# Optimization experiments

Measured on AMD Instinct MI355X. Metric: run time of the kernel, lower is better.

Reference implementation:

```python
import jax, jax.numpy as jnp
import numpy as np

N = 20000       # nodes
E = 320000      # edges
D_IN = 128
H = 512
OUT = 7
EPS = 1e-5


def setup_inputs() -> dict:
    key = jax.random.key(0)
    ks = jax.random.split(key, 16)
    def lin(k, fan_in, fan_out):
        bound = 1.0 / np.sqrt(fan_in)
        kw, kb = jax.random.split(k)
        W = jax.random.uniform(kw, (fan_in, fan_out), jnp.float32, -bound, bound)
        b = jax.random.uniform(kb, (fan_out,), jnp.float32, -bound, bound)
        return W, b
    x = jax.random.normal(ks[0], (N, D_IN), jnp.float32)
    edge_index = jax.random.randint(ks[1], (2, E), 0, N, dtype=jnp.int64)
    W1, b1 = lin(ks[2], D_IN, H)
    W2, b2 = lin(ks[3], H, H)
    W3, b3 = lin(ks[4], H, H)
    W4, b4 = lin(ks[5], H, H)
    ln_gamma = jnp.ones((H,), jnp.float32)
    ln_beta = jnp.zeros((H,), jnp.float32)
    W_out, b_out = lin(ks[6], H, OUT)
    return {"x": x, "edge_index": edge_index,
            "W1": W1, "b1": b1, "W2": W2, "b2": b2,
            "W3": W3, "b3": b3, "W4": W4, "b4": b4,
            "ln_gamma": ln_gamma, "ln_beta": ln_beta,
            "W_out": W_out, "b_out": b_out}


def _gcn_layer(x, W, b, src, dst, dinv):
    # transform, then symmetric-normalized gather/scatter-add (PyG GCNConv)
    h = x @ W                                    # [N, H]
    norm = dinv[src] * dinv[dst]                 # [E+N]
    msg = h[src] * norm[:, None]                 # gather + scale
    agg = jax.ops.segment_sum(msg, dst, num_segments=N)
    return agg + b


def reference(x, edge_index, W1, b1, W2, b2, W3, b3, W4, b4,
              ln_gamma, ln_beta, W_out, b_out):
    loops = jnp.arange(N, dtype=edge_index.dtype)
    src = jnp.concatenate([edge_index[0], loops])  # A + I self loops
    dst = jnp.concatenate([edge_index[1], loops])
    deg = jax.ops.segment_sum(jnp.ones_like(src, dtype=x.dtype), dst,
                              num_segments=N)
    dinv = jnp.where(deg > 0, jax.lax.rsqrt(deg), 0.0)

    def ln(h):
        mu = h.mean(-1, keepdims=True)
        var = h.var(-1, keepdims=True)
        return (h - mu) * jax.lax.rsqrt(var + EPS) * ln_gamma + ln_beta

    for W, b in ((W1, b1), (W2, b2), (W3, b3), (W4, b4)):
        x = jax.nn.relu(ln(_gcn_layer(x, W, b, src, dst, dinv)))
    g = x.mean(axis=0)           # mean pool over nodes -> [H]
    # dropout is identity in eval mode
    return g @ W_out + b_out     # [OUT]
```

## Files before the change

kernel.cpp:

```cpp
#include <hip/hip_runtime.h>

#define HID 512
#define OUTD 7
#define EPSV 1e-5f
#define PR 32

typedef __attribute__((ext_vector_type(8))) short bf16x8;
typedef __attribute__((ext_vector_type(4))) float f32x4;
typedef __attribute__((ext_vector_type(2))) float f32x2;
typedef unsigned short ushort_t;
typedef unsigned int uint_t;
typedef unsigned char uchar_t;

__device__ __forceinline__ ushort_t f2bf(float f) {
    uint_t u = __float_as_uint(f);
    u = (u + 0x7fffu + ((u >> 16) & 1u)) >> 16;
    return (ushort_t)u;
}
__device__ __forceinline__ float bflo(uint_t u) { return __uint_as_float(u << 16); }
__device__ __forceinline__ float bfhi(uint_t u) { return __uint_as_float(u & 0xffff0000u); }

__device__ __forceinline__ void dec4(uint_t v, float* f) {
    f32x2 p0 = __builtin_amdgcn_cvt_pk_f32_fp8(v, false);
    f32x2 p1 = __builtin_amdgcn_cvt_pk_f32_fp8(v, true);
    f[0] = p0.x; f[1] = p0.y; f[2] = p1.x; f[3] = p1.y;
}
__device__ __forceinline__ uint_t enc4(float a, float b, float c, float d) {
    uint_t r = __builtin_amdgcn_cvt_pk_fp8_f32(a, b, 0, false);
    r = __builtin_amdgcn_cvt_pk_fp8_f32(c, d, r, true);
    return r;
}

__device__ __forceinline__ void gload_lds16(const ushort_t* g, ushort_t* l) {
    __builtin_amdgcn_global_load_lds(
        (const __attribute__((address_space(1))) uint_t*)g,
        (__attribute__((address_space(3))) uint_t*)l, 16, 0, 0);
}

__global__ __launch_bounds__(256) void deg_wtrans(
        const int* __restrict__ dst, int* __restrict__ deg, int E, int degB,
        const float* __restrict__ W0, const float* __restrict__ W1,
        const float* __restrict__ W2, const float* __restrict__ W3,
        ushort_t* __restrict__ T0, ushort_t* __restrict__ T1,
        ushort_t* __restrict__ T2, ushort_t* __restrict__ T3) {
    __shared__ ushort_t tile[32][33];
    if ((int)blockIdx.x < degB) {
        int e = blockIdx.x * 256 + threadIdx.x;
        if (e < E) atomicAdd(&deg[dst[e]], 1);
        return;
    }
    int id = blockIdx.x - degB;
    const float* W; ushort_t* T; int K;
    if (id < 64)       { W = W0; T = T0; K = 128; }
    else if (id < 320) { W = W1; T = T1; K = 512; id -= 64; }
    else if (id < 576) { W = W2; T = T2; K = 512; id -= 320; }
    else               { W = W3; T = T3; K = 512; id -= 576; }
    const int tn = id & 15;
    const int tk = id >> 4;
    const int t = threadIdx.x;
    const int r = t >> 3;
    const int c4 = (t & 7) * 4;
    const float4 v = *(const float4*)&W[(size_t)(tk * 32 + r) * HID + tn * 32 + c4];
    tile[r][c4 + 0] = f2bf(v.x); tile[r][c4 + 1] = f2bf(v.y);
    tile[r][c4 + 2] = f2bf(v.z); tile[r][c4 + 3] = f2bf(v.w);
    __syncthreads();
    ushort4 ov = make_ushort4(tile[c4 + 0][r], tile[c4 + 1][r],
                              tile[c4 + 2][r], tile[c4 + 3][r]);
    *(ushort4*)&T[(size_t)(tn * 32 + r) * K + tk * 32 + c4] = ov;
}


__global__ void scan1(const int* __restrict__ deg, int* __restrict__ off,
                      int* __restrict__ partial, float* __restrict__ dinv, int N) {
    __shared__ int s[256];
    const int t = threadIdx.x;
    const int i = blockIdx.x * 256 + t;
    int d = (i < N) ? deg[i] : 0;
    if (i < N) dinv[i] = rsqrtf((float)(d + 1));
    s[t] = d;
    __syncthreads();
#pragma unroll
    for (int ofs = 1; ofs < 256; ofs <<= 1) {
        int v = (t >= ofs) ? s[t - ofs] : 0;
        __syncthreads();
        s[t] += v;
        __syncthreads();
    }
    if (i < N) off[i] = s[t] - d;
    if (t == 255) partial[blockIdx.x] = s[255];
}

__global__ void scan23(int* __restrict__ off, const int* __restrict__ partial,
                       int* __restrict__ cursor, int N, int E, int nb) {
    __shared__ int s[256];
    __shared__ int ex[256];
    const int t = threadIdx.x;
    int d = (t < nb) ? partial[t] : 0;
    s[t] = d;
    __syncthreads();
#pragma unroll
    for (int ofs = 1; ofs < 256; ofs <<= 1) {
        int v = (t >= ofs) ? s[t - ofs] : 0;
        __syncthreads();
        s[t] += v;
        __syncthreads();
    }
    ex[t] = s[t] - d;
    __syncthreads();
    int i = blockIdx.x * 256 + t;
    if (i < N) {
        int v = off[i] + ex[i >> 8];
        off[i] = v;
        cursor[i] = v;
    } else if (i == N) {
        off[N] = E;
    }
}


__global__ void fill_cvt(const int* __restrict__ src, const int* __restrict__ dst,
                         int* __restrict__ cursor, int* __restrict__ srcs, int E,
                         const float* __restrict__ x, const float* __restrict__ dinv,
                         ushort_t* __restrict__ xb, int pairs) {
    int i = blockIdx.x * blockDim.x + threadIdx.x;
    if (i < E) { int p = atomicAdd(&cursor[dst[i]], 1); srcs[p] = src[i]; return; }
    i -= E;
    if (i < pairs) {
        float dr = dinv[i >> 6];
        float a = x[2 * i] * dr, b = x[2 * i + 1] * dr;
        uint_t d = __builtin_amdgcn_cvt_pk_fp8_f32(a, b, 0, false);
        xb[i] = (ushort_t)(d & 0xffffu);
    }
}


__global__ __launch_bounds__(256) void csr_agg_512(
        const uchar_t* __restrict__ xs, const int* __restrict__ off,
        const int* __restrict__ srcs, const float* __restrict__ dinv,
        ushort_t* __restrict__ ax, int N) {
    int gtid = blockIdx.x * 256 + threadIdx.x;
    int r = gtid >> 6, lane = gtid & 63;
    if (r >= N) return;
    const int half = lane >> 5, l32 = lane & 31;
    const uint4* xb = (const uint4*)xs;
    float a[16];
    if (half == 0) {
        uint4 v = xb[(size_t)r * 32 + l32];
        dec4(v.x, a); dec4(v.y, a + 4); dec4(v.z, a + 8); dec4(v.w, a + 12);
    } else {
#pragma unroll
        for (int q = 0; q < 16; q++) a[q] = 0.f;
    }
    int e = off[r];
    const int e1 = off[r + 1];
    for (; e + 8 <= e1; e += 8) {
        int si[4]; uint4 vi[4];
#pragma unroll
        for (int j = 0; j < 4; j++) si[j] = srcs[e + 2 * j + half];
#pragma unroll
        for (int j = 0; j < 4; j++) vi[j] = xb[(size_t)si[j] * 32 + l32];
#pragma unroll
        for (int j = 0; j < 4; j++) {
            float f[16];
            dec4(vi[j].x, f); dec4(vi[j].y, f + 4); dec4(vi[j].z, f + 8); dec4(vi[j].w, f + 12);
#pragma unroll
            for (int q = 0; q < 16; q++) a[q] += f[q];
        }
    }
    for (; e < e1; e += 2) {
        int idx = e + half;
        bool valid = idx < e1;
        int s = srcs[valid ? idx : e];
        uint4 v = xb[(size_t)s * 32 + l32];
        if (!valid) { v.x = 0; v.y = 0; v.z = 0; v.w = 0; }
        float f[16];
        dec4(v.x, f); dec4(v.y, f + 4); dec4(v.z, f + 8); dec4(v.w, f + 12);
#pragma unroll
        for (int q = 0; q < 16; q++) a[q] += f[q];
    }
#pragma unroll
    for (int q = 0; q < 16; q++) a[q] += __shfl_xor(a[q], 32);
    {
        float dr = dinv[r];
        const int b = half * 8;
        uint_t w0 = (uint_t)f2bf(a[b + 0] * dr) | ((uint_t)f2bf(a[b + 1] * dr) << 16);
        uint_t w1 = (uint_t)f2bf(a[b + 2] * dr) | ((uint_t)f2bf(a[b + 3] * dr) << 16);
        uint_t w2 = (uint_t)f2bf(a[b + 4] * dr) | ((uint_t)f2bf(a[b + 5] * dr) << 16);
        uint_t w3 = (uint_t)f2bf(a[b + 6] * dr) | ((uint_t)f2bf(a[b + 7] * dr) << 16);
        ((uint4*)ax)[(size_t)r * 64 + l32 * 2 + half] = make_uint4(w0, w1, w2, w3);
    }
}

__global__ __launch_bounds__(256) void csr_agg_128(
        const uchar_t* __restrict__ xs, const int* __restrict__ off,
        const int* __restrict__ srcs, const float* __restrict__ dinv,
        ushort_t* __restrict__ ax, int N) {
    int gtid = blockIdx.x * 256 + threadIdx.x;
    int r = gtid >> 6, lane = gtid & 63;
    if (r >= N) return;
    const int sub = lane >> 3, l8 = lane & 7;
    const uint4* xb = (const uint4*)xs;
    float a[16];
    if (sub == 0) {
        uint4 v = xb[(size_t)r * 8 + l8];
        dec4(v.x, a); dec4(v.y, a + 4); dec4(v.z, a + 8); dec4(v.w, a + 12);
    } else {
#pragma unroll
        for (int q = 0; q < 16; q++) a[q] = 0.f;
    }
    const int e1 = off[r + 1];
    for (int e = off[r]; e < e1; e += 8) {
        int idx = e + sub;
        bool valid = idx < e1;
        int s = srcs[valid ? idx : e];
        uint4 v = xb[(size_t)s * 8 + l8];
        if (!valid) { v.x = 0; v.y = 0; v.z = 0; v.w = 0; }
        float f[16];
        dec4(v.x, f); dec4(v.y, f + 4); dec4(v.z, f + 8); dec4(v.w, f + 12);
#pragma unroll
        for (int q = 0; q < 16; q++) a[q] += f[q];
    }
#pragma unroll
    for (int q = 0; q < 16; q++) a[q] += __shfl_xor(a[q], 8);
#pragma unroll
    for (int q = 0; q < 16; q++) a[q] += __shfl_xor(a[q], 16);
#pragma unroll
    for (int q = 0; q < 16; q++) a[q] += __shfl_xor(a[q], 32);
    if (sub < 2) {
        float dr = dinv[r];
        const int b = sub * 8;
        uint_t w0 = (uint_t)f2bf(a[b + 0] * dr) | ((uint_t)f2bf(a[b + 1] * dr) << 16);
        uint_t w1 = (uint_t)f2bf(a[b + 2] * dr) | ((uint_t)f2bf(a[b + 3] * dr) << 16);
        uint_t w2 = (uint_t)f2bf(a[b + 4] * dr) | ((uint_t)f2bf(a[b + 5] * dr) << 16);
        uint_t w3 = (uint_t)f2bf(a[b + 6] * dr) | ((uint_t)f2bf(a[b + 7] * dr) << 16);
        ((uint4*)ax)[(size_t)r * 16 + l8 * 2 + sub] = make_uint4(w0, w1, w2, w3);
    }
}


template<int POOL>
__global__ __launch_bounds__(256) void gemm_ln(
        const ushort_t* __restrict__ A, const ushort_t* __restrict__ Wt,
        const float* __restrict__ bias, const float* __restrict__ gamma,
        const float* __restrict__ beta, const float* __restrict__ dinv,
        uchar_t* __restrict__ out8, float* __restrict__ pbuf, int M, int K) {
    __shared__ __align__(16) ushort_t AsL[32 * 64];
    __shared__ __align__(16) ushort_t BsL[512 * 64];
    __shared__ float sred[4][32][2];
    const int t = threadIdx.x;
    const int wave = t >> 6, lane = t & 63;
    const int m0 = blockIdx.x * 32;
    const int wn = wave * 128;
    const int quad = lane >> 4, l16 = lane & 15;
    const int srow = lane >> 3;
    const int schunk = (lane & 7) ^ srow;
    const int sw = (l16 & 7) << 4;

    f32x4 acc[2][8];
#pragma unroll
    for (int im = 0; im < 2; im++)
#pragma unroll
        for (int jn = 0; jn < 8; jn++) acc[im][jn] = (f32x4){0.f, 0.f, 0.f, 0.f};

    for (int k0 = 0; k0 < K; k0 += 64) {
        {
            int gm = m0 + wave * 8 + srow;
            if (gm >= M) gm = M - 1;
            gload_lds16(A + (size_t)gm * K + k0 + (schunk << 3), AsL + wave * 512);
        }
#pragma unroll
        for (int j = 0; j < 16; j++) {
            const int c = wave * 16 + j;
            gload_lds16(Wt + (size_t)(8 * c + srow) * K + k0 + (schunk << 3),
                        BsL + c * 512);
        }
        __syncthreads();
#pragma unroll
        for (int kk = 0; kk < 2; kk++) {
            const int kb = (kk * 4 + quad) << 4;
            bf16x8 af[2], bfr[8];
#pragma unroll
            for (int jn = 0; jn < 8; jn++)
                bfr[jn] = *(const bf16x8*)((const char*)BsL
                              + (wn + jn * 16 + l16) * 128 + (kb ^ sw));
#pragma unroll
            for (int im = 0; im < 2; im++)
                af[im] = *(const bf16x8*)((const char*)AsL
                              + (im * 16 + l16) * 128 + (kb ^ sw));
#pragma unroll
            for (int im = 0; im < 2; im++)
#pragma unroll
                for (int jn = 0; jn < 8; jn++)
                    acc[im][jn] = __builtin_amdgcn_mfma_f32_16x16x32_bf16(
                                      bfr[jn], af[im], acc[im][jn], 0, 0, 0);
        }
        __syncthreads();
    }

    float4 bias4[8];
#pragma unroll
    for (int jn = 0; jn < 8; jn++)
        bias4[jn] = *(const float4*)&bias[wn + jn * 16 + quad * 4];

#pragma unroll
    for (int im = 0; im < 2; im++) {
        float s = 0.f, q = 0.f;
#pragma unroll
        for (int jn = 0; jn < 8; jn++) {
#pragma unroll
            for (int rg = 0; rg < 4; rg++) {
                float h = acc[im][jn][rg] + ((const float*)&bias4[jn])[rg];
                s += h; q += h * h;
            }
        }
        s += __shfl_xor(s, 16); s += __shfl_xor(s, 32);
        q += __shfl_xor(q, 16); q += __shfl_xor(q, 32);
        if (quad == 0) { sred[wave][im * 16 + l16][0] = s; sred[wave][im * 16 + l16][1] = q; }
    }
    __syncthreads();

    float cacc[8][4];
    if (POOL) {
#pragma unroll
        for (int jn = 0; jn < 8; jn++)
#pragma unroll
            for (int rg = 0; rg < 4; rg++) cacc[jn][rg] = 0.f;
    }

#pragma unroll
    for (int im = 0; im < 2; im++) {
        const int row = im * 16 + l16;
        const float st = sred[0][row][0] + sred[1][row][0] + sred[2][row][0] + sred[3][row][0];
        const float qt = sred[0][row][1] + sred[1][row][1] + sred[2][row][1] + sred[3][row][1];
        const float mu = st * (1.0f / HID);
        const float var = qt * (1.0f / HID) - mu * mu;
        const float rs = rsqrtf(var + EPSV);
        const int gm = m0 + row;
        const bool ok = gm < M;
        float dr = 0.f;
        if (!POOL) dr = ok ? dinv[gm] : 0.f;
#pragma unroll
        for (int jn = 0; jn < 8; jn++) {
            const float4 g4 = *(const float4*)&gamma[wn + jn * 16 + quad * 4];
            const float4 b4 = *(const float4*)&beta[wn + jn * 16 + quad * 4];
            float o[4];
#pragma unroll
            for (int rg = 0; rg < 4; rg++) {
                float h = acc[im][jn][rg] + ((const float*)&bias4[jn])[rg];
                o[rg] = fmaxf((h - mu) * rs * ((const float*)&g4)[rg]
                              + ((const float*)&b4)[rg], 0.f);
            }
            if (POOL) {
#pragma unroll
                for (int rg = 0; rg < 4; rg++) cacc[jn][rg] += ok ? o[rg] : 0.f;
            } else if (ok) {
                *(uint_t*)(out8 + (size_t)gm * HID + wn + jn * 16 + quad * 4) =
                    enc4(o[0] * dr, o[1] * dr, o[2] * dr, o[3] * dr);
            }
        }
    }

    if (POOL) {
#pragma unroll
        for (int jn = 0; jn < 8; jn++)
#pragma unroll
            for (int rg = 0; rg < 4; rg++) {
                float v = cacc[jn][rg];
                v += __shfl_xor(v, 1); v += __shfl_xor(v, 2);
                v += __shfl_xor(v, 4); v += __shfl_xor(v, 8);
                cacc[jn][rg] = v;
            }
        if (l16 == 0) {
#pragma unroll
            for (int jn = 0; jn < 8; jn++) {
                float4 v = make_float4(cacc[jn][0], cacc[jn][1], cacc[jn][2], cacc[jn][3]);
                *(float4*)&pbuf[(size_t)blockIdx.x * HID + wn + jn * 16 + quad * 4] = v;
            }
        }
    }
}


__global__ __launch_bounds__(256) void pool_reduce(
        const float* __restrict__ pbuf, float* __restrict__ pbuf2, int NB) {
    const int t = threadIdx.x;
    const int b = blockIdx.x;
    const int R = (NB + PR - 1) / PR;
    float2 s = make_float2(0.f, 0.f);
    for (int u = 0; u < R; u++) {
        int r = b * R + u;
        if (r < NB) {
            const float2 v = ((const float2*)(pbuf + (size_t)r * HID))[t];
            s.x += v.x; s.y += v.y;
        }
    }
    ((float2*)(pbuf2 + (size_t)b * HID))[t] = s;
}


__global__ void out_kernel(const float* __restrict__ pbuf2, const float* __restrict__ Wout,
                           const float* __restrict__ bout, float* __restrict__ out, int N) {
    __shared__ float red[256];
    int t = threadIdx.x;
    float g0 = 0.f, g1 = 0.f;
#pragma unroll
    for (int p = 0; p < PR; p += 8) {
#pragma unroll
        for (int u = 0; u < 8; u++) {
            const float2 v = ((const float2*)(pbuf2 + (size_t)(p + u) * HID))[t];
            g0 += v.x; g1 += v.y;
        }
    }
    float invn = 1.0f / (float)N;
    for (int o = 0; o < OUTD; o++) {
        float pr = g0 * Wout[(2 * t) * OUTD + o] + g1 * Wout[(2 * t + 1) * OUTD + o];
        red[t] = pr;
        __syncthreads();
        for (int sft = 128; sft > 0; sft >>= 1) {
            if (t < sft) red[t] += red[t + sft];
            __syncthreads();
        }
        if (t == 0) out[o] = red[0] * invn + bout[o];
        __syncthreads();
    }
}


extern "C" void kernel_launch(void* const* d_in, const int* in_sizes, int n_in,
                              void* d_out, int out_size, void* d_ws, size_t ws_size,
                              hipStream_t stream) {
    const float* x  = (const float*)d_in[0];
    const int*   ei = (const int*)d_in[1];
    const int N = in_sizes[0] / 128;
    const int E = in_sizes[1] / 2;
    const int* src = ei;
    const int* dst = ei + E;
    const float* Ws[4] = {(const float*)d_in[2], (const float*)d_in[4],
                          (const float*)d_in[6], (const float*)d_in[8]};
    const float* bs[4] = {(const float*)d_in[3], (const float*)d_in[5],
                          (const float*)d_in[7], (const float*)d_in[9]};
    const float* gamma = (const float*)d_in[10];
    const float* beta  = (const float*)d_in[11];
    const float* Wout  = (const float*)d_in[12];
    const float* bout  = (const float*)d_in[13];
    float* out = (float*)d_out;

    const int NBM = (N + 31) / 32;

    char* p = (char*)d_ws;
    ushort_t* axb = (ushort_t*)p;  p += sizeof(ushort_t) * (size_t)N * HID;
    uchar_t*  ho8 = (uchar_t*)p;   p += (size_t)N * HID;
    uchar_t*  xb8 = ho8;
    ushort_t* Wt[4];
    Wt[0] = (ushort_t*)p;          p += sizeof(ushort_t) * 128 * HID;
    Wt[1] = (ushort_t*)p;          p += sizeof(ushort_t) * HID * HID;
    Wt[2] = (ushort_t*)p;          p += sizeof(ushort_t) * HID * HID;
    Wt[3] = (ushort_t*)p;          p += sizeof(ushort_t) * HID * HID;
    float* dinv  = (float*)p;      p += sizeof(float) * N;
    float* pbuf  = (float*)p;      p += sizeof(float) * (size_t)(NBM + 4) * HID;
    float* pbuf2 = (float*)p;      p += sizeof(float) * PR * HID;
    int* deg    = (int*)p;         p += sizeof(int) * N;
    int* off    = (int*)p;         p += sizeof(int) * (N + 4);
    int* cursor = (int*)p;         p += sizeof(int) * N;
    int* partial= (int*)p;         p += sizeof(int) * 256;
    int* srcs   = (int*)p;

    const int nb = (N + 255) / 256;
    const int degB = (E + 255) / 256;

    hipMemsetAsync(deg, 0, sizeof(int) * N, stream);
    deg_wtrans<<<degB + 832, 256, 0, stream>>>(dst, deg, E, degB,
                                               Ws[0], Ws[1], Ws[2], Ws[3],
                                               Wt[0], Wt[1], Wt[2], Wt[3]);
    scan1<<<nb, 256, 0, stream>>>(deg, off, partial, dinv, N);
    scan23<<<(N + 256) / 256, 256, 0, stream>>>(off, partial, cursor, N, E, nb);
    {
        int pairs = N * 64;
        int tot = E + pairs;
        fill_cvt<<<(tot + 255) / 256, 256, 0, stream>>>(src, dst, cursor, srcs, E,
                                                        x, dinv, (ushort_t*)xb8, pairs);
    }

    for (int l = 0; l < 4; l++) {
        const int K = (l == 0) ? 128 : HID;
        if (l == 0)
            csr_agg_128<<<(N * 64 + 255) / 256, 256, 0, stream>>>(xb8, off, srcs, dinv, axb, N);
        else
            csr_agg_512<<<(N * 64 + 255) / 256, 256, 0, stream>>>(ho8, off, srcs, dinv, axb, N);
        if (l < 3)
            gemm_ln<0><<<NBM, 256, 0, stream>>>(axb, Wt[l], bs[l], gamma, beta, dinv,
                                                ho8, pbuf, N, K);
        else
            gemm_ln<1><<<NBM, 256, 0, stream>>>(axb, Wt[l], bs[l], gamma, beta, dinv,
                                                ho8, pbuf, N, K);
    }
    pool_reduce<<<PR, 256, 0, stream>>>(pbuf, pbuf2, NBM);
    out_kernel<<<1, 256, 0, stream>>>(pbuf2, Wout, bout, out, N);
}
```

Baseline: 426.2 us.

## Pre-swizzle weights to MFMA fragment layout and split aggregation by column chunks

The transposed bf16 weights are now stored in a fragment-major layout, so the GEMM reads B operands straight from global memory/L2 instead of staging 512x64 tiles in LDS. LDS is used only for A, with 128-wide K steps and K as a template parameter. The 512-wide aggregation is split over a 2D grid of four column chunks, with eight edge groups per wave and shuffle reductions. This cuts LDS footprint and barrier traffic and should raise occupancy, but B loads now come from cache on every kk step, and each gather row is touched by four blocks.

```diff
diff --git a/kernel.cpp b/kernel.cpp
--- a/kernel.cpp
+++ b/kernel.cpp
@@ -66,7 +66,12 @@
     __syncthreads();
     ushort4 ov = make_ushort4(tile[c4 + 0][r], tile[c4 + 1][r],
                               tile[c4 + 2][r], tile[c4 + 3][r]);
-    *(ushort4*)&T[(size_t)(tn * 32 + r) * K + tk * 32 + c4] = ov;
+    const int n   = tn * 32 + r;
+    const int n16 = n >> 4, l16n = n & 15;
+    const int kb  = tk * 32 + c4;
+    const int kc  = kb >> 3, k8 = kb & 7;
+    size_t idx = ((((size_t)n16 * (K >> 3) + kc) << 4) + l16n) * 8 + k8;
+    *(ushort4*)&T[idx] = ov;
 }
 
 
@@ -134,18 +139,21 @@
 }
 
 
-__global__ __launch_bounds__(256) void csr_agg_512(
+__global__ __launch_bounds__(256) void csr_agg_col(
         const uchar_t* __restrict__ xs, const int* __restrict__ off,
         const int* __restrict__ srcs, const float* __restrict__ dinv,
         ushort_t* __restrict__ ax, int N) {
-    int gtid = blockIdx.x * 256 + threadIdx.x;
-    int r = gtid >> 6, lane = gtid & 63;
+    const int r = blockIdx.x * 4 + (threadIdx.x >> 6);
     if (r >= N) return;
-    const int half = lane >> 5, l32 = lane & 31;
+    const int c = blockIdx.y;
+    const int lane = threadIdx.x & 63;
+    const int eg = lane >> 3;
+    const int sc = lane & 7;
     const uint4* xb = (const uint4*)xs;
+    const int cbase = c * 8 + sc;
     float a[16];
-    if (half == 0) {
-        uint4 v = xb[(size_t)r * 32 + l32];
+    if (eg == 0) {
+        uint4 v = xb[(size_t)r * 32 + cbase];
         dec4(v.x, a); dec4(v.y, a + 4); dec4(v.z, a + 8); dec4(v.w, a + 12);
     } else {
 #pragma unroll
@@ -153,25 +161,23 @@
     }
     int e = off[r];
     const int e1 = off[r + 1];
-    for (; e + 8 <= e1; e += 8) {
-        int si[4]; uint4 vi[4];
-#pragma unroll
-        for (int j = 0; j < 4; j++) si[j] = srcs[e + 2 * j + half];
-#pragma unroll
-        for (int j = 0; j < 4; j++) vi[j] = xb[(size_t)si[j] * 32 + l32];
-#pragma unroll
-        for (int j = 0; j < 4; j++) {
-            float f[16];
-            dec4(vi[j].x, f); dec4(vi[j].y, f + 4); dec4(vi[j].z, f + 8); dec4(vi[j].w, f + 12);
-#pragma unroll
-            for (int q = 0; q < 16; q++) a[q] += f[q];
-        }
-    }
-    for (; e < e1; e += 2) {
-        int idx = e + half;
+    for (; e + 16 <= e1; e += 16) {
+        int s0 = srcs[e + eg], s1 = srcs[e + 8 + eg];
+        uint4 v0 = xb[(size_t)s0 * 32 + cbase];
+        uint4 v1 = xb[(size_t)s1 * 32 + cbase];
+        float f[16];
+        dec4(v0.x, f); dec4(v0.y, f + 4); dec4(v0.z, f + 8); dec4(v0.w, f + 12);
+#pragma unroll
+        for (int q = 0; q < 16; q++) a[q] += f[q];
+        dec4(v1.x, f); dec4(v1.y, f + 4); dec4(v1.z, f + 8); dec4(v1.w, f + 12);
+#pragma unroll
+        for (int q = 0; q < 16; q++) a[q] += f[q];
+    }
+    for (; e < e1; e += 8) {
+        int idx = e + eg;
         bool valid = idx < e1;
         int s = srcs[valid ? idx : e];
-        uint4 v = xb[(size_t)s * 32 + l32];
+        uint4 v = xb[(size_t)s * 32 + cbase];
         if (!valid) { v.x = 0; v.y = 0; v.z = 0; v.w = 0; }
         float f[16];
         dec4(v.x, f); dec4(v.y, f + 4); dec4(v.z, f + 8); dec4(v.w, f + 12);
@@ -179,15 +185,21 @@
         for (int q = 0; q < 16; q++) a[q] += f[q];
     }
 #pragma unroll
+    for (int q = 0; q < 16; q++) a[q] += __shfl_xor(a[q], 8);
+#pragma unroll
+    for (int q = 0; q < 16; q++) a[q] += __shfl_xor(a[q], 16);
+#pragma unroll
     for (int q = 0; q < 16; q++) a[q] += __shfl_xor(a[q], 32);
-    {
-        float dr = dinv[r];
-        const int b = half * 8;
+    if (lane < 16) {
+        const float dr = dinv[r];
+        const int b = (lane >> 3) * 8;
+        const int osc = lane & 7;
         uint_t w0 = (uint_t)f2bf(a[b + 0] * dr) | ((uint_t)f2bf(a[b + 1] * dr) << 16);
         uint_t w1 = (uint_t)f2bf(a[b + 2] * dr) | ((uint_t)f2bf(a[b + 3] * dr) << 16);
         uint_t w2 = (uint_t)f2bf(a[b + 4] * dr) | ((uint_t)f2bf(a[b + 5] * dr) << 16);
         uint_t w3 = (uint_t)f2bf(a[b + 6] * dr) | ((uint_t)f2bf(a[b + 7] * dr) << 16);
-        ((uint4*)ax)[(size_t)r * 64 + l32 * 2 + half] = make_uint4(w0, w1, w2, w3);
+        ((uint4*)ax)[(size_t)r * 64 + c * 16 + osc * 2 + (lane >> 3)] =
+            make_uint4(w0, w1, w2, w3);
     }
 }
 
@@ -238,23 +250,20 @@
 }
 
 
-template<int POOL>
+template<int POOL, int K>
 __global__ __launch_bounds__(256) void gemm_ln(
-        const ushort_t* __restrict__ A, const ushort_t* __restrict__ Wt,
+        const ushort_t* __restrict__ A, const ushort_t* __restrict__ Wf,
         const float* __restrict__ bias, const float* __restrict__ gamma,
         const float* __restrict__ beta, const float* __restrict__ dinv,
-        uchar_t* __restrict__ out8, float* __restrict__ pbuf, int M, int K) {
-    __shared__ __align__(16) ushort_t AsL[32 * 64];
-    __shared__ __align__(16) ushort_t BsL[512 * 64];
+        uchar_t* __restrict__ out8, float* __restrict__ pbuf, int M) {
+    __shared__ __align__(16) ushort_t AsL[32 * 128];
     __shared__ float sred[4][32][2];
     const int t = threadIdx.x;
     const int wave = t >> 6, lane = t & 63;
     const int m0 = blockIdx.x * 32;
     const int wn = wave * 128;
     const int quad = lane >> 4, l16 = lane & 15;
-    const int srow = lane >> 3;
-    const int schunk = (lane & 7) ^ srow;
-    const int sw = (l16 & 7) << 4;
+    const int K8 = K >> 3;
 
     f32x4 acc[2][8];
 #pragma unroll
@@ -262,31 +271,33 @@
 #pragma unroll
         for (int jn = 0; jn < 8; jn++) acc[im][jn] = (f32x4){0.f, 0.f, 0.f, 0.f};
 
-    for (int k0 = 0; k0 < K; k0 += 64) {
-        {
-            int gm = m0 + wave * 8 + srow;
+    const int srow4 = lane >> 4;
+    const int ckd   = lane & 15;
+#pragma unroll 1
+    for (int k0 = 0; k0 < K; k0 += 128) {
+#pragma unroll
+        for (int j = 0; j < 2; j++) {
+            const int rr = wave * 8 + j * 4 + srow4;
+            int gm = m0 + rr;
             if (gm >= M) gm = M - 1;
-            gload_lds16(A + (size_t)gm * K + k0 + (schunk << 3), AsL + wave * 512);
-        }
-#pragma unroll
-        for (int j = 0; j < 16; j++) {
-            const int c = wave * 16 + j;
-            gload_lds16(Wt + (size_t)(8 * c + srow) * K + k0 + (schunk << 3),
-                        BsL + c * 512);
-        }
-        __syncthreads();
-#pragma unroll
-        for (int kk = 0; kk < 2; kk++) {
-            const int kb = (kk * 4 + quad) << 4;
-            bf16x8 af[2], bfr[8];
+            const int cks = ckd ^ (rr & 7);
+            gload_lds16(A + (size_t)gm * K + k0 + cks * 8,
+                        AsL + (size_t)wave * 1024 + j * 512);
+        }
+        __syncthreads();
+#pragma unroll
+        for (int kk = 0; kk < 4; kk++) {
+            const int kc = (k0 >> 3) + kk * 4 + quad;
+            bf16x8 bfr[8], af[2];
 #pragma unroll
             for (int jn = 0; jn < 8; jn++)
-                bfr[jn] = *(const bf16x8*)((const char*)BsL
-                              + (wn + jn * 16 + l16) * 128 + (kb ^ sw));
+                bfr[jn] = *(const bf16x8*)
+                    &Wf[((((size_t)(wave * 8 + jn) * K8 + kc) << 4) + l16) * 8];
+            const int ckr = (kk * 4 + quad) ^ (l16 & 7);
 #pragma unroll
             for (int im = 0; im < 2; im++)
                 af[im] = *(const bf16x8*)((const char*)AsL
-                              + (im * 16 + l16) * 128 + (kb ^ sw));
+                              + (im * 16 + l16) * 256 + ckr * 16);
 #pragma unroll
             for (int im = 0; im < 2; im++)
 #pragma unroll
@@ -481,18 +492,21 @@
                                                         x, dinv, (ushort_t*)xb8, pairs);
     }
 
+    const dim3 aggGrid((N + 3) / 4, 4);
     for (int l = 0; l < 4; l++) {
-        const int K = (l == 0) ? 128 : HID;
         if (l == 0)
             csr_agg_128<<<(N * 64 + 255) / 256, 256, 0, stream>>>(xb8, off, srcs, dinv, axb, N);
         else
-            csr_agg_512<<<(N * 64 + 255) / 256, 256, 0, stream>>>(ho8, off, srcs, dinv, axb, N);
-        if (l < 3)
-            gemm_ln<0><<<NBM, 256, 0, stream>>>(axb, Wt[l], bs[l], gamma, beta, dinv,
-                                                ho8, pbuf, N, K);
+            csr_agg_col<<<aggGrid, 256, 0, stream>>>(ho8, off, srcs, dinv, axb, N);
+        if (l == 0)
+            gemm_ln<0, 128><<<NBM, 256, 0, stream>>>(axb, Wt[0], bs[0], gamma, beta, dinv,
+                                                     ho8, pbuf, N);
+        else if (l < 3)
+            gemm_ln<0, 512><<<NBM, 256, 0, stream>>>(axb, Wt[l], bs[l], gamma, beta, dinv,
+                                                     ho8, pbuf, N);
         else
-            gemm_ln<1><<<NBM, 256, 0, stream>>>(axb, Wt[l], bs[l], gamma, beta, dinv,
-                                                ho8, pbuf, N, K);
+            gemm_ln<1, 512><<<NBM, 256, 0, stream>>>(axb, Wt[l], bs[l], gamma, beta, dinv,
+                                                     ho8, pbuf, N);
     }
     pool_reduce<<<PR, 256, 0, stream>>>(pbuf, pbuf2, NBM);
     out_kernel<<<1, 256, 0, stream>>>(pbuf2, Wout, bout, out, N);
```

Result: slower. 472.1 us (+10.8%).
